# Performance work log

Measured on AMD Instinct MI355X. Metric: run time of the kernel, lower is better.

The kernel has to match this reference:

```python
import jax, jax.numpy as jnp
import numpy as np
from math import ceil, log2

IN_W, IN_F = 8, 4
VAR_W, VAR_F = 16, 8
OUT_W, OUT_F = 8, 4
LUT_POW = 5
SQRT2_FIX = int(np.floor(np.sqrt(2.0) * 2 ** (VAR_W - 1)))  # Q1.(W-1) sqrt(2)


def make_isqrt_lut(lut_pow: int, width: int) -> np.ndarray:
    # lut[i] ~= 1/sqrt(u) for normalized u = 1 + i/2^lut_pow in [1,2), Q1.(width-1)
    i = np.arange(2 ** lut_pow, dtype=np.float64)
    vals = np.floor((1.0 / np.sqrt(1.0 + i / 2 ** lut_pow)) * 2 ** (width - 1))
    return vals.astype(np.int32)


def integer_floor_quantizer(x, width, frac):
    s = jnp.float32(2.0 ** frac)
    xi = jnp.floor(x * s)
    xi = jnp.clip(xi, -(2 ** (width - 1)), 2 ** (width - 1) - 1)
    return xi / s


def isqrt_int(x_int, lut):
    # vectorized fixed-point inverse sqrt: x_int is QW.F int32 >= 0,
    # returns int in [0, 2^W-1] representing 1/sqrt(x_int/2^F) in QW.F
    W, F, P = VAR_W, VAR_F, LUT_POW
    bits = jnp.left_shift(jnp.int32(1), jnp.arange(W, dtype=jnp.int32))
    msb = jnp.sum((x_int[..., None] >= bits).astype(jnp.int32), axis=-1) - 1
    msb = jnp.maximum(msb, 0)
    x_red = jnp.left_shift(x_int, (W - 1) - msb)  # MSB aligned to bit W-1, u in [1,2)
    idx = jnp.right_shift(x_red, W - 1 - P) & ((1 << P) - 1)  # top P frac bits of u
    lv = lut[idx].astype(jnp.int32)
    e = 3 * F - msb  # result = lut * 2^(e/2) / 2^(W-1)
    e2 = e // 2
    odd = e - 2 * e2
    lv = jnp.where(odd == 1, jnp.right_shift(lv * SQRT2_FIX, W - 1), lv)
    sh = (W - 1) - e2
    res = jnp.where(sh >= 0,
                    jnp.right_shift(lv, jnp.maximum(sh, 0)),
                    jnp.left_shift(lv, jnp.maximum(-sh, 0)))
    res = jnp.where(x_int == 0, (1 << W) - 1, res)  # saturate on zero variance
    return jnp.clip(res, 0, (1 << W) - 1)


def fixed_signed_cast(x, width, frac):
    xi = jnp.floor(x * jnp.float32(2.0 ** frac))
    xi = jnp.clip(xi, -(2 ** (width - 1)), 2 ** (width - 1) - 1)
    x_float = xi / jnp.float32(2.0 ** frac)
    x_uint = jnp.mod(xi.astype(jnp.int32), 1 << width)  # two's-complement bits
    return x_float, x_uint


def setup_inputs() -> dict:
    key = jax.random.key(0)
    x = jax.random.normal(key, (64, 128, 64, 64), dtype=jnp.float32)
    lut = jnp.asarray(make_isqrt_lut(LUT_POW, VAR_W))
    return {"x": x, "isqrt_lut": lut}


def reference(x, isqrt_lut):
    mu = jnp.mean(x, axis=(1, 2, 3), keepdims=True)
    mu = integer_floor_quantizer(mu, IN_W, IN_F)
    var = jnp.mean((x - mu) ** 2, axis=(1, 2, 3), keepdims=True)
    var = integer_floor_quantizer(var, VAR_W, VAR_F)
    var_int = (var * 2 ** VAR_F).astype(jnp.int32)
    inv_sqrt_int = isqrt_int(var_int, isqrt_lut)
    inv_sqrt = inv_sqrt_int.astype(jnp.float32) / jnp.float32(2.0 ** VAR_F)
    inv_sqrt = integer_floor_quantizer(inv_sqrt, VAR_W, VAR_F)
    norm = (x - mu) * inv_sqrt
    norm_float, norm_uint = fixed_signed_cast(norm, OUT_W, OUT_F)
    return norm_float, norm_uint
```

## Files before the change

### kernel.cpp

```cpp
#include <hip/hip_runtime.h>
#include <math.h>


#define NSAMP 64
#define SELEMS (128 * 64 * 64)
#define RB_PER 16
#define RBLOCKS (NSAMP * RB_PER)
#define RTHREADS 256
#define RVEC (SELEMS / RB_PER / 4)

#define N2THREADS 512

typedef float f32x4 __attribute__((ext_vector_type(4)));

__global__ __launch_bounds__(RTHREADS)
void gn_reduce(const float* __restrict__ x, double* __restrict__ part) {
    int blk = blockIdx.x;
    int samp = blk >> 4;
    int sub  = blk & 15;
    const f32x4* xs = reinterpret_cast<const f32x4*>(x)
                    + (size_t)samp * (SELEMS / 4)
                    + (size_t)sub * RVEC;
    double s = 0.0, s2 = 0.0;
    for (int i = threadIdx.x; i < RVEC; i += RTHREADS) {
        f32x4 v = xs[i];
        double a = v.x, b = v.y, c = v.z, d = v.w;
        s  += (a + b) + (c + d);
        s2 += (a * a + b * b) + (c * c + d * d);
    }
    __shared__ double sh1[RTHREADS];
    __shared__ double sh2[RTHREADS];
    int tid = threadIdx.x;
    sh1[tid] = s; sh2[tid] = s2;
    __syncthreads();
    for (int off = RTHREADS / 2; off > 0; off >>= 1) {
        if (tid < off) { sh1[tid] += sh1[tid + off]; sh2[tid] += sh2[tid + off]; }
        __syncthreads();
    }
    if (tid == 0) { part[blk * 2] = sh1[0]; part[blk * 2 + 1] = sh2[0]; }
}

__device__ __forceinline__ void compute_params(const double* __restrict__ part,
                                               const int* __restrict__ lut,
                                               int samp, float* mu_out, float* is_out) {
    double sum = 0.0, sum2 = 0.0;
    #pragma unroll
    for (int i = 0; i < RB_PER; ++i) {
        sum  += part[(samp * RB_PER + i) * 2];
        sum2 += part[(samp * RB_PER + i) * 2 + 1];
    }
    const double invN = 1.0 / (double)SELEMS;
    double mean = sum * invN;
    double mi = floor(mean * 16.0);
    mi = fmin(fmax(mi, -128.0), 127.0);
    double mu = mi / 16.0;
    double var = sum2 * invN - 2.0 * mu * mean + mu * mu;
    if (var < 0.0) var = 0.0;
    double vq = floor(var * 256.0);
    vq = fmin(fmax(vq, -32768.0), 32767.0);
    int var_int = (int)vq;

    int res;
    if (var_int <= 0) {
        res = 65535;
    } else {
        int msb = 31 - __clz(var_int);
        int x_red = var_int << (15 - msb);
        int idx = (x_red >> 10) & 31;
        int lv = lut[idx];
        int e = 24 - msb;
        int e2 = e >> 1;
        if (e & 1) lv = (lv * 46340) >> 15;
        res = lv >> (15 - e2);
        if (res > 65535) res = 65535;
    }
    if (res > 32767) res = 32767;

    *mu_out = (float)mu;
    *is_out = (float)res * (1.0f / 256.0f);
}

__global__ __launch_bounds__(N2THREADS)
void gn_norm(const float* __restrict__ x, const double* __restrict__ part,
             const int* __restrict__ lut,
             float* __restrict__ outf, float* __restrict__ outu) {
    int blk  = blockIdx.x;
    int samp = blk >> 4;
    int sub  = blk & 15;

    float mu, is;
    compute_params(part, lut, samp, &mu, &is);

    size_t base = (size_t)samp * (SELEMS / 4) + (size_t)sub * RVEC;
    const f32x4* xs = reinterpret_cast<const f32x4*>(x) + base;
    f32x4* of = reinterpret_cast<f32x4*>(outf) + base;
    f32x4* ou = reinterpret_cast<f32x4*>(outu) + base;

    for (int i = RVEC - N2THREADS + (int)threadIdx.x; i >= 0; i -= N2THREADS) {
        f32x4 v = xs[i];
        f32x4 rf, ru;
        {
            float d = (v.x - mu) * is;
            float t = floorf(d * 16.0f);
            t = fminf(fmaxf(t, -128.0f), 127.0f);
            rf.x = t * 0.0625f;
            ru.x = (float)(((int)t) & 255);
        }
        {
            float d = (v.y - mu) * is;
            float t = floorf(d * 16.0f);
            t = fminf(fmaxf(t, -128.0f), 127.0f);
            rf.y = t * 0.0625f;
            ru.y = (float)(((int)t) & 255);
        }
        {
            float d = (v.z - mu) * is;
            float t = floorf(d * 16.0f);
            t = fminf(fmaxf(t, -128.0f), 127.0f);
            rf.z = t * 0.0625f;
            ru.z = (float)(((int)t) & 255);
        }
        {
            float d = (v.w - mu) * is;
            float t = floorf(d * 16.0f);
            t = fminf(fmaxf(t, -128.0f), 127.0f);
            rf.w = t * 0.0625f;
            ru.w = (float)(((int)t) & 255);
        }
        __builtin_nontemporal_store(rf, of + i);
        __builtin_nontemporal_store(ru, ou + i);
    }
}

extern "C" void kernel_launch(void* const* d_in, const int* in_sizes, int n_in,
                              void* d_out, int out_size, void* d_ws, size_t ws_size,
                              hipStream_t stream) {
    const float* x = (const float*)d_in[0];
    const int* lut = (const int*)d_in[1];
    float* outf = (float*)d_out;
    float* outu = outf + (size_t)NSAMP * SELEMS;
    double* part = (double*)d_ws;

    gn_reduce<<<RBLOCKS, RTHREADS, 0, stream>>>(x, part);
    gn_norm<<<RBLOCKS, N2THREADS, 0, stream>>>(x, part, lut, outf, outu);
}
```

Before: 83.79 us.

## Fuse reduce and normalize into one cooperative kernel caching input on-chip

Replaces the two-pass reduce-then-normalize pair with a single cooperative kernel of 512 blocks. Each block loads its chunk once, keeps part of it in LDS (9 vectors per thread, 72 KB) and the rest in registers (23 float4 per thread), and computes per-wave partial sums. It then does a grid-wide sync and normalizes from the on-chip copy, avoiding a second read of the input from HBM. The cost is heavy register and LDS pressure, which needs every block to be resident at once, plus the overhead of a grid sync. If the cooperative launch fails, it falls back to the old two-kernel path.

```diff
diff --git a/kernel.cpp b/kernel.cpp
--- a/kernel.cpp
+++ b/kernel.cpp
@@ -1,53 +1,54 @@
 #include <hip/hip_runtime.h>
+#include <hip/hip_cooperative_groups.h>
 #include <math.h>
+
+namespace cg = cooperative_groups;
 
 
 #define NSAMP 64
 #define SELEMS (128 * 64 * 64)
-#define RB_PER 16
-#define RBLOCKS (NSAMP * RB_PER)
-#define RTHREADS 256
-#define RVEC (SELEMS / RB_PER / 4)
-
-#define N2THREADS 512
+#define BLOCKS 512
+#define THREADS 512
+#define BLK_PER_SAMP 8
+#define CHUNK4 (SELEMS / BLK_PER_SAMP / 4)
+#define LDS_ITERS 9
+#define REG_ITERS 23
 
 typedef float f32x4 __attribute__((ext_vector_type(4)));
 
-__global__ __launch_bounds__(RTHREADS)
-void gn_reduce(const float* __restrict__ x, double* __restrict__ part) {
-    int blk = blockIdx.x;
-    int samp = blk >> 4;
-    int sub  = blk & 15;
-    const f32x4* xs = reinterpret_cast<const f32x4*>(x)
-                    + (size_t)samp * (SELEMS / 4)
-                    + (size_t)sub * RVEC;
-    double s = 0.0, s2 = 0.0;
-    for (int i = threadIdx.x; i < RVEC; i += RTHREADS) {
-        f32x4 v = xs[i];
-        double a = v.x, b = v.y, c = v.z, d = v.w;
-        s  += (a + b) + (c + d);
-        s2 += (a * a + b * b) + (c * c + d * d);
-    }
-    __shared__ double sh1[RTHREADS];
-    __shared__ double sh2[RTHREADS];
-    int tid = threadIdx.x;
-    sh1[tid] = s; sh2[tid] = s2;
-    __syncthreads();
-    for (int off = RTHREADS / 2; off > 0; off >>= 1) {
-        if (tid < off) { sh1[tid] += sh1[tid + off]; sh2[tid] += sh2[tid + off]; }
-        __syncthreads();
-    }
-    if (tid == 0) { part[blk * 2] = sh1[0]; part[blk * 2 + 1] = sh2[0]; }
+struct QPair { float f, u; };
+
+__device__ __forceinline__ QPair quant1(float v, float mu, float is) {
+    float d = (v - mu) * is;
+    float t = floorf(d * 16.0f);
+    t = fminf(fmaxf(t, -128.0f), 127.0f);
+    QPair q;
+    q.f = t * 0.0625f;
+    q.u = (float)(((int)t) & 255);
+    return q;
+}
+
+__device__ __forceinline__ void quant4(f32x4 v, float mu, float is,
+                                       f32x4* rf, f32x4* ru) {
+    QPair a = quant1(v.x, mu, is);
+    QPair b = quant1(v.y, mu, is);
+    QPair c = quant1(v.z, mu, is);
+    QPair d = quant1(v.w, mu, is);
+    f32x4 f, u;
+    f.x = a.f; f.y = b.f; f.z = c.f; f.w = d.f;
+    u.x = a.u; u.y = b.u; u.z = c.u; u.w = d.u;
+    *rf = f; *ru = u;
 }
 
 __device__ __forceinline__ void compute_params(const double* __restrict__ part,
                                                const int* __restrict__ lut,
-                                               int samp, float* mu_out, float* is_out) {
+                                               int samp, int nper,
+                                               float* mu_out, float* is_out) {
     double sum = 0.0, sum2 = 0.0;
-    #pragma unroll
-    for (int i = 0; i < RB_PER; ++i) {
-        sum  += part[(samp * RB_PER + i) * 2];
-        sum2 += part[(samp * RB_PER + i) * 2 + 1];
+    int jb = samp * nper;
+    for (int j = 0; j < nper; ++j) {
+        sum  += part[(jb + j) * 2];
+        sum2 += part[(jb + j) * 2 + 1];
     }
     const double invN = 1.0 / (double)SELEMS;
     double mean = sum * invN;
@@ -80,6 +81,113 @@
     *is_out = (float)res * (1.0f / 256.0f);
 }
 
+__global__ __launch_bounds__(THREADS, 4)
+void gn_fused(const float* __restrict__ x, double* __restrict__ part,
+              const int* __restrict__ lut,
+              float* __restrict__ outf, float* __restrict__ outu) {
+    int blk  = blockIdx.x;
+    int samp = blk >> 3;
+    int sub  = blk & 7;
+    int t    = threadIdx.x;
+    size_t base4 = (size_t)samp * (SELEMS / 4) + (size_t)sub * CHUNK4;
+    const f32x4* xs = reinterpret_cast<const f32x4*>(x) + base4;
+
+    __shared__ f32x4 lds4[LDS_ITERS * THREADS];
+    __shared__ float psh[2];
+
+    f32x4 r[REG_ITERS];
+    double s = 0.0, s2 = 0.0;
+
+    #pragma unroll
+    for (int i = 0; i < LDS_ITERS; ++i) {
+        f32x4 v = xs[i * THREADS + t];
+        lds4[i * THREADS + t] = v;
+        double a = v.x, b = v.y, c = v.z, d = v.w;
+        s  += (a + b) + (c + d);
+        s2 += (a * a + b * b) + (c * c + d * d);
+    }
+    #pragma unroll
+    for (int i = 0; i < REG_ITERS; ++i) {
+        f32x4 v = xs[(LDS_ITERS + i) * THREADS + t];
+        r[i] = v;
+        double a = v.x, b = v.y, c = v.z, d = v.w;
+        s  += (a + b) + (c + d);
+        s2 += (a * a + b * b) + (c * c + d * d);
+    }
+
+    #pragma unroll
+    for (int off = 32; off > 0; off >>= 1) {
+        s  += __shfl_down(s,  off, 64);
+        s2 += __shfl_down(s2, off, 64);
+    }
+    int wid = t >> 6, lane = t & 63;
+    if (lane == 0) {
+        part[(blk * 8 + wid) * 2]     = s;
+        part[(blk * 8 + wid) * 2 + 1] = s2;
+    }
+
+    cg::this_grid().sync();
+
+    if (t == 0) {
+        float mu, is;
+        compute_params(part, lut, samp, 64, &mu, &is);
+        psh[0] = mu; psh[1] = is;
+    }
+    __syncthreads();
+    float mu = psh[0], is = psh[1];
+
+    f32x4* of = reinterpret_cast<f32x4*>(outf) + base4;
+    f32x4* ou = reinterpret_cast<f32x4*>(outu) + base4;
+
+    #pragma unroll
+    for (int i = 0; i < LDS_ITERS; ++i) {
+        f32x4 v = lds4[i * THREADS + t];
+        f32x4 rf, ru;
+        quant4(v, mu, is, &rf, &ru);
+        __builtin_nontemporal_store(rf, of + i * THREADS + t);
+        __builtin_nontemporal_store(ru, ou + i * THREADS + t);
+    }
+    #pragma unroll
+    for (int i = 0; i < REG_ITERS; ++i) {
+        f32x4 rf, ru;
+        quant4(r[i], mu, is, &rf, &ru);
+        __builtin_nontemporal_store(rf, of + (LDS_ITERS + i) * THREADS + t);
+        __builtin_nontemporal_store(ru, ou + (LDS_ITERS + i) * THREADS + t);
+    }
+}
+
+#define RB_PER 16
+#define RBLOCKS (NSAMP * RB_PER)
+#define RTHREADS 256
+#define RVEC (SELEMS / RB_PER / 4)
+#define N2THREADS 512
+
+__global__ __launch_bounds__(RTHREADS)
+void gn_reduce(const float* __restrict__ x, double* __restrict__ part) {
+    int blk = blockIdx.x;
+    int samp = blk >> 4;
+    int sub  = blk & 15;
+    const f32x4* xs = reinterpret_cast<const f32x4*>(x)
+                    + (size_t)samp * (SELEMS / 4) + (size_t)sub * RVEC;
+    double s = 0.0, s2 = 0.0;
+    for (int i = threadIdx.x; i < RVEC; i += RTHREADS) {
+        f32x4 v = xs[i];
+        double a = v.x, b = v.y, c = v.z, d = v.w;
+        s  += (a + b) + (c + d);
+        s2 += (a * a + b * b) + (c * c + d * d);
+    }
+    __shared__ double sh1[RTHREADS];
+    __shared__ double sh2[RTHREADS];
+    int tid = threadIdx.x;
+    sh1[tid] = s; sh2[tid] = s2;
+    __syncthreads();
+    for (int off = RTHREADS / 2; off > 0; off >>= 1) {
+        if (tid < off) { sh1[tid] += sh1[tid + off]; sh2[tid] += sh2[tid + off]; }
+        __syncthreads();
+    }
+    if (tid == 0) { part[blk * 2] = sh1[0]; part[blk * 2 + 1] = sh2[0]; }
+}
+
 __global__ __launch_bounds__(N2THREADS)
 void gn_norm(const float* __restrict__ x, const double* __restrict__ part,
              const int* __restrict__ lut,
@@ -87,46 +195,16 @@
     int blk  = blockIdx.x;
     int samp = blk >> 4;
     int sub  = blk & 15;
-
     float mu, is;
-    compute_params(part, lut, samp, &mu, &is);
-
+    compute_params(part, lut, samp, RB_PER, &mu, &is);
     size_t base = (size_t)samp * (SELEMS / 4) + (size_t)sub * RVEC;
     const f32x4* xs = reinterpret_cast<const f32x4*>(x) + base;
     f32x4* of = reinterpret_cast<f32x4*>(outf) + base;
     f32x4* ou = reinterpret_cast<f32x4*>(outu) + base;
-
     for (int i = RVEC - N2THREADS + (int)threadIdx.x; i >= 0; i -= N2THREADS) {
         f32x4 v = xs[i];
         f32x4 rf, ru;
-        {
-            float d = (v.x - mu) * is;
-            float t = floorf(d * 16.0f);
-            t = fminf(fmaxf(t, -128.0f), 127.0f);
-            rf.x = t * 0.0625f;
-            ru.x = (float)(((int)t) & 255);
-        }
-        {
-            float d = (v.y - mu) * is;
-            float t = floorf(d * 16.0f);
-            t = fminf(fmaxf(t, -128.0f), 127.0f);
-            rf.y = t * 0.0625f;
-            ru.y = (float)(((int)t) & 255);
-        }
-        {
-            float d = (v.z - mu) * is;
-            float t = floorf(d * 16.0f);
-            t = fminf(fmaxf(t, -128.0f), 127.0f);
-            rf.z = t * 0.0625f;
-            ru.z = (float)(((int)t) & 255);
-        }
-        {
-            float d = (v.w - mu) * is;
-            float t = floorf(d * 16.0f);
-            t = fminf(fmaxf(t, -128.0f), 127.0f);
-            rf.w = t * 0.0625f;
-            ru.w = (float)(((int)t) & 255);
-        }
+        quant4(v, mu, is, &rf, &ru);
         __builtin_nontemporal_store(rf, of + i);
         __builtin_nontemporal_store(ru, ou + i);
     }
@@ -141,6 +219,13 @@
     float* outu = outf + (size_t)NSAMP * SELEMS;
     double* part = (double*)d_ws;
 
-    gn_reduce<<<RBLOCKS, RTHREADS, 0, stream>>>(x, part);
-    gn_norm<<<RBLOCKS, N2THREADS, 0, stream>>>(x, part, lut, outf, outu);
-}
+    void* args[] = { (void*)&x, (void*)&part, (void*)&lut,
+                     (void*)&outf, (void*)&outu };
+    hipError_t e = hipLaunchCooperativeKernel((const void*)gn_fused,
+                                              dim3(BLOCKS), dim3(THREADS),
+                                              args, 0, stream);
+    if (e != hipSuccess) {
+        gn_reduce<<<RBLOCKS, RTHREADS, 0, stream>>>(x, part);
+        gn_norm<<<RBLOCKS, N2THREADS, 0, stream>>>(x, part, lut, outf, outu);
+    }
+}
```

After: 142.1 us. 1.7x slower.
